# Optimization experiments

Measured on AMD Instinct MI355X. Metric: run time of the kernel, lower is better.

Reference implementation:

```python
import jax, jax.numpy as jnp
import numpy as np

HIDDEN = 1280
HEADS = 16
HEAD_DIM = HIDDEN // HEADS  # 80
TOTAL = 8192
N_CHUNKS = 8


def rotate_half(x):
    x1, x2 = jnp.split(x, 2, axis=-1)
    return jnp.concatenate([-x2, x1], axis=-1)


def setup_inputs() -> dict:
    key = jax.random.key(0)
    ks = jax.random.split(key, 7)
    hidden_states = jax.random.normal(ks[0], (TOTAL, HIDDEN), dtype=jnp.float32)
    cos = jax.random.uniform(ks[1], (TOTAL, HEAD_DIM), dtype=jnp.float32)
    sin = jax.random.uniform(ks[2], (TOTAL, HEAD_DIM), dtype=jnp.float32)
    s = 1.0 / np.sqrt(HIDDEN)
    w_qkv = jax.random.normal(ks[3], (HIDDEN, 3 * HIDDEN), dtype=jnp.float32) * s
    b_qkv = jax.random.normal(ks[4], (3 * HIDDEN,), dtype=jnp.float32) * 0.01
    w_proj = jax.random.normal(ks[5], (HIDDEN, HIDDEN), dtype=jnp.float32) * s
    b_proj = jax.random.normal(ks[6], (HIDDEN,), dtype=jnp.float32) * 0.01
    return {"hidden_states": hidden_states, "cos": cos, "sin": sin,
            "w_qkv": w_qkv, "b_qkv": b_qkv, "w_proj": w_proj,
            "b_proj": b_proj, "n_chunks": N_CHUNKS}


def reference(hidden_states, cos, sin, w_qkv, b_qkv, w_proj, b_proj, n_chunks):
    T, D = hidden_states.shape
    C = int(n_chunks)
    L = T // C  # equal-length chunks (block-diagonal varlen attention)
    H, hd = HEADS, HEAD_DIM
    scale = hd ** -0.5

    qkv = hidden_states @ w_qkv + b_qkv                    # [T, 3D]
    q, k, v = jnp.split(qkv, 3, axis=-1)
    # [C, L, H, hd]
    q = q.reshape(C, L, H, hd)
    k = k.reshape(C, L, H, hd)
    v = v.reshape(C, L, H, hd)
    cos_c = cos.reshape(C, L, 1, hd)
    sin_c = sin.reshape(C, L, 1, hd)
    q = q * cos_c + rotate_half(q) * sin_c
    k = k * cos_c + rotate_half(k) * sin_c

    # block-diagonal attention: each chunk attends only within itself
    scores = jnp.einsum('clhd,cmhd->chlm', q, k) * scale   # [C, H, L, L]
    weights = jax.nn.softmax(scores.astype(jnp.float32), axis=-1).astype(v.dtype)
    attn = jnp.einsum('chlm,cmhd->clhd', weights, v)       # [C, L, H, hd]
    attn = attn.reshape(T, D)
    return attn @ w_proj + b_proj
```

## Files before the change

### kernel.cpp

```cpp
#include <hip/hip_runtime.h>

#define T_TOK 8192
#define D_HID 1280
#define H_    16
#define HD_   80
#define C_    8
#define L_    1024
#define N3_   3840
#define QPAD  96

typedef _Float16 f16;
typedef __attribute__((ext_vector_type(8))) _Float16 h8;
typedef __attribute__((ext_vector_type(4))) float f32x4;

__global__ __launch_bounds__(256) void convert_x(const float* __restrict__ x,
                                                 f16* __restrict__ y) {
  const int g = blockIdx.x * 256 + threadIdx.x;
  const float4 v = ((const float4*)x)[g];
  f16 o[4] = {(f16)v.x, (f16)v.y, (f16)v.z, (f16)v.w};
  ((uint2*)y)[g] = *(const uint2*)o;
}

__global__ __launch_bounds__(256) void convert_w_t(const float* __restrict__ W,
                                                   f16* __restrict__ Wt,
                                                   int K, int N) {
  __shared__ float tile[32][33];
  const int n0 = blockIdx.x * 32, k0 = blockIdx.y * 32;
  const int c = threadIdx.x & 31, r0 = threadIdx.x >> 5;
#pragma unroll
  for (int it = 0; it < 4; ++it) {
    const int r = r0 + it * 8;
    tile[r][c] = W[(size_t)(k0 + r) * N + n0 + c];
  }
  __syncthreads();
#pragma unroll
  for (int it = 0; it < 4; ++it) {
    const int r = r0 + it * 8;
    Wt[(size_t)(n0 + r) * K + k0 + c] = (f16)tile[c][r];
  }
}

__device__ __forceinline__ void stage_rows(const f16* __restrict__ gbase, int K,
                                           f16* sdst, int nchunks, int tid) {
  for (int s0 = 0; s0 < nchunks; s0 += 256) {
    const int s = s0 + tid;
    const int row = s >> 3;
    const int part = (s & 7) ^ (row & 7);
    const f16* gp = gbase + (size_t)row * K + part * 8;
    __builtin_amdgcn_global_load_lds(
        (const __attribute__((address_space(1))) void*)gp,
        (__attribute__((address_space(3))) void*)(sdst + s * 8),
        16, 0, 0);
  }
}

__device__ __forceinline__ h8 fragld64(const f16* s, int row, int c) {
  const int slot = c ^ (row & 7);
  return *(const h8*)&s[row * 64 + slot * 8];
}

__global__ __launch_bounds__(256, 2) void gemm_f16(
    const f16* __restrict__ A, const f16* __restrict__ B,
    const float* __restrict__ bias,
    float* __restrict__ Cf, f16* __restrict__ Ch,
    int M, int N, int K) {
  __shared__ f16 sA[128 * 64], sB[256 * 64];
  const int tid = threadIdx.x;
  const int wave = tid >> 6, lane = tid & 63;
  const int quad = lane >> 4, ln = lane & 15;
  const int bm = blockIdx.y * 128, bn = blockIdx.x * 256;
  const int wm = (wave >> 1) * 64, wn = (wave & 1) * 128;

  f32x4 acc[4][8];
#pragma unroll
  for (int i = 0; i < 4; ++i)
#pragma unroll
    for (int j = 0; j < 8; ++j) acc[i][j] = (f32x4){0.f, 0.f, 0.f, 0.f};

  for (int k0 = 0; k0 < K; k0 += 64) {
    __syncthreads();
    stage_rows(A + (size_t)bm * K + k0, K, sA, 128 * 8, tid);
    stage_rows(B + (size_t)bn * K + k0, K, sB, 256 * 8, tid);
    __syncthreads();

#pragma unroll
    for (int ks = 0; ks < 2; ++ks) {
      h8 af[4], bf[8];
#pragma unroll
      for (int i = 0; i < 4; ++i) af[i] = fragld64(sA, wm + i * 16 + ln, ks * 4 + quad);
#pragma unroll
      for (int j = 0; j < 8; ++j) bf[j] = fragld64(sB, wn + j * 16 + ln, ks * 4 + quad);
#pragma unroll
      for (int i = 0; i < 4; ++i)
#pragma unroll
        for (int j = 0; j < 8; ++j)
          acc[i][j] = __builtin_amdgcn_mfma_f32_16x16x32_f16(af[i], bf[j], acc[i][j], 0, 0, 0);
    }
  }

  float bv[8];
#pragma unroll
  for (int j = 0; j < 8; ++j) bv[j] = bias[bn + wn + j * 16 + ln];
#pragma unroll
  for (int i = 0; i < 4; ++i)
#pragma unroll
    for (int j = 0; j < 8; ++j)
#pragma unroll
      for (int r = 0; r < 4; ++r) {
        const int row = bm + wm + i * 16 + quad * 4 + r;
        const int col = bn + wn + j * 16 + ln;
        const float val = acc[i][j][r] + bv[j];
        if (Ch) Ch[(size_t)row * N + col] = (f16)val;
        else    Cf[(size_t)row * N + col] = val;
      }
}

__global__ __launch_bounds__(256) void rope_convert(
    const f16* __restrict__ qkv, const float* __restrict__ cosb,
    const float* __restrict__ sinb, f16* __restrict__ Qb, f16* __restrict__ Kb) {
  const int tid = threadIdx.x;
  const int wave = tid >> 6, lane = tid & 63;
  const int t = blockIdx.x * 4 + wave;
  const size_t rowb = (size_t)t * N3_;
  const float qscale = 0.11180339887498949f;
#pragma unroll
  for (int u = 0; u < 5; ++u) {
    const int g = u * 64 + lane;
    const int e = g * 8;
    const int d = e % HD_;
    const int h = (e % D_HID) / HD_;
    const bool isK = e >= D_HID;
    const bool lo = d < 40;
    const int pe = lo ? e + 40 : e - 40;
    f16 v[8], p[8];
    *(int4*)v = *(const int4*)(qkv + rowb + e);
    *(int4*)p = *(const int4*)(qkv + rowb + pe);
    const float4 cs0 = *(const float4*)(cosb + (size_t)t * HD_ + d);
    const float4 cs1 = *(const float4*)(cosb + (size_t)t * HD_ + d + 4);
    const float4 sn0 = *(const float4*)(sinb + (size_t)t * HD_ + d);
    const float4 sn1 = *(const float4*)(sinb + (size_t)t * HD_ + d + 4);
    const float cs[8] = {cs0.x, cs0.y, cs0.z, cs0.w, cs1.x, cs1.y, cs1.z, cs1.w};
    const float sn[8] = {sn0.x, sn0.y, sn0.z, sn0.w, sn1.x, sn1.y, sn1.z, sn1.w};
    f16 o[8];
#pragma unroll
    for (int j = 0; j < 8; ++j) {
      const float pv = lo ? -(float)p[j] : (float)p[j];
      const float ov = (float)v[j] * cs[j] + pv * sn[j];
      o[j] = (f16)(isK ? ov : ov * qscale);
    }
    *(int4*)((isK ? Kb : Qb) + ((size_t)h * T_TOK + t) * QPAD + d) = *(const int4*)o;
  }
  {
    const int qk = lane >> 5, h = (lane >> 1) & 15, half = lane & 1;
    f16* dst = (qk ? Kb : Qb) + ((size_t)h * T_TOK + t) * QPAD + 80 + half * 8;
    *(int4*)dst = make_int4(0, 0, 0, 0);
  }
}

__global__ __launch_bounds__(256) void vt_convert(const f16* __restrict__ qkv,
                                                  f16* __restrict__ Vt) {
  __shared__ f16 tl[HD_][136];
  const int h = blockIdx.x & 15;
  const int t0 = (blockIdx.x >> 4) * 128;
  const int tid = threadIdx.x;
#pragma unroll
  for (int it = 0; it < 5; ++it) {
    const int e = tid + it * 256;
    const int t = e / 10, pc = e % 10;
    int4 v = *(const int4*)(qkv + (size_t)(t0 + t) * N3_ + 2 * D_HID + h * HD_ + pc * 8);
    f16 tmp[8];
    *(int4*)tmp = v;
#pragma unroll
    for (int u = 0; u < 8; ++u) tl[pc * 8 + u][t] = tmp[u];
  }
  __syncthreads();
#pragma unroll
  for (int it = 0; it < 5; ++it) {
    const int e = tid + it * 256;
    const int d = e >> 4, pt = e & 15;
    *(int4*)(Vt + ((size_t)h * HD_ + d) * T_TOK + t0 + pt * 8) = *(const int4*)&tl[d][pt * 8];
  }
}

__global__ __launch_bounds__(256, 2) void attn_flash(
    const f16* __restrict__ Qb, const f16* __restrict__ Kb,
    const f16* __restrict__ Vt, f16* __restrict__ Oa) {
  __shared__ f16 Ps[4][64][72];
  const int tid = threadIdx.x;
  const int wave = tid >> 6, lane = tid & 63;
  const int quad = lane >> 4, ln = lane & 15;
  const int h = blockIdx.x & 15;
  const int qb = (blockIdx.x >> 4) & 3;
  const int c = blockIdx.x >> 6;
  const int t0 = c * L_ + qb * 256 + wave * 64;
  const size_t hb = (size_t)h * T_TOK;

  h8 aq[4][3];
#pragma unroll
  for (int i = 0; i < 4; ++i)
#pragma unroll
    for (int ks = 0; ks < 3; ++ks)
      aq[i][ks] = *(const h8*)(Qb + (hb + t0 + i * 16 + ln) * QPAD + ks * 32 + quad * 8);

  f32x4 o[4][5];
  float lsum[4][4];
#pragma unroll
  for (int i = 0; i < 4; ++i) {
#pragma unroll
    for (int jn = 0; jn < 5; ++jn) o[i][jn] = (f32x4){0.f, 0.f, 0.f, 0.f};
#pragma unroll
    for (int r = 0; r < 4; ++r) lsum[i][r] = 0.f;
  }

  for (int kb = 0; kb < 16; ++kb) {
    const int kt0 = c * L_ + kb * 64;
#pragma unroll
    for (int j = 0; j < 4; ++j) {
      h8 bk[3];
#pragma unroll
      for (int ks = 0; ks < 3; ++ks)
        bk[ks] = *(const h8*)(Kb + (hb + kt0 + j * 16 + ln) * QPAD + ks * 32 + quad * 8);
      f32x4 s[4];
#pragma unroll
      for (int i = 0; i < 4; ++i) s[i] = (f32x4){0.f, 0.f, 0.f, 0.f};
      __builtin_amdgcn_s_setprio(1);
#pragma unroll
      for (int ks = 0; ks < 3; ++ks)
#pragma unroll
        for (int i = 0; i < 4; ++i)
          s[i] = __builtin_amdgcn_mfma_f32_16x16x32_f16(aq[i][ks], bk[ks], s[i], 0, 0, 0);
      __builtin_amdgcn_s_setprio(0);
#pragma unroll
      for (int i = 0; i < 4; ++i)
#pragma unroll
        for (int r = 0; r < 4; ++r) {
          const float p = __expf(s[i][r]);
          lsum[i][r] += p;
          Ps[wave][i * 16 + quad * 4 + r][j * 16 + ln] = (f16)p;
        }
    }
#pragma unroll
    for (int ks = 0; ks < 2; ++ks) {
      h8 ap[4];
#pragma unroll
      for (int i = 0; i < 4; ++i)
        ap[i] = *(const h8*)&Ps[wave][i * 16 + ln][ks * 32 + quad * 8];
#pragma unroll
      for (int jn = 0; jn < 5; ++jn) {
        const h8 bv = *(const h8*)(Vt + ((size_t)h * HD_ + jn * 16 + ln) * T_TOK
                                   + kt0 + ks * 32 + quad * 8);
        __builtin_amdgcn_s_setprio(1);
#pragma unroll
        for (int i = 0; i < 4; ++i)
          o[i][jn] = __builtin_amdgcn_mfma_f32_16x16x32_f16(ap[i], bv, o[i][jn], 0, 0, 0);
        __builtin_amdgcn_s_setprio(0);
      }
    }
  }

#pragma unroll
  for (int i = 0; i < 4; ++i)
#pragma unroll
    for (int r = 0; r < 4; ++r) {
      float s = lsum[i][r];
#pragma unroll
      for (int off = 1; off < 16; off <<= 1) s += __shfl_xor(s, off);
      lsum[i][r] = 1.f / s;
    }

#pragma unroll
  for (int i = 0; i < 4; ++i)
#pragma unroll
    for (int r = 0; r < 4; ++r) {
      const int t = t0 + i * 16 + quad * 4 + r;
      const float inv = lsum[i][r];
#pragma unroll
      for (int jn = 0; jn < 5; ++jn)
        Oa[(size_t)t * D_HID + h * HD_ + jn * 16 + ln] = (f16)(o[i][jn][r] * inv);
    }
}

extern "C" void kernel_launch(void* const* d_in, const int* in_sizes, int n_in,
                              void* d_out, int out_size, void* d_ws, size_t ws_size,
                              hipStream_t stream) {
  (void)in_sizes; (void)n_in; (void)out_size; (void)ws_size;
  const float* x      = (const float*)d_in[0];
  const float* cosb   = (const float*)d_in[1];
  const float* sinb   = (const float*)d_in[2];
  const float* w_qkv  = (const float*)d_in[3];
  const float* b_qkv  = (const float*)d_in[4];
  const float* w_proj = (const float*)d_in[5];
  const float* b_proj = (const float*)d_in[6];
  float* out = (float*)d_out;

  char* ws = (char*)d_ws;
  f16* qkv_h  = (f16*)(ws);
  f16* attn_h = (f16*)(ws);
  f16* x_h    = (f16*)(ws + 62914560);
  f16* Qb     = (f16*)(ws + 62914560);
  f16* Kb     = (f16*)(ws + 88080384);
  f16* Vt     = (f16*)(ws + 113246208);
  f16* wq_t   = (f16*)(ws + 134217728);
  f16* wp_t   = (f16*)(ws + 144048128);

  convert_x<<<(T_TOK * D_HID / 4) / 256, 256, 0, stream>>>(x, x_h);
  convert_w_t<<<dim3(N3_ / 32, D_HID / 32), 256, 0, stream>>>(w_qkv, wq_t, D_HID, N3_);
  convert_w_t<<<dim3(D_HID / 32, D_HID / 32), 256, 0, stream>>>(w_proj, wp_t, D_HID, D_HID);
  gemm_f16<<<dim3(N3_ / 256, T_TOK / 128), 256, 0, stream>>>(
      x_h, wq_t, b_qkv, nullptr, qkv_h, T_TOK, N3_, D_HID);
  rope_convert<<<T_TOK / 4, 256, 0, stream>>>(qkv_h, cosb, sinb, Qb, Kb);
  vt_convert<<<H_ * (T_TOK / 128), 256, 0, stream>>>(qkv_h, Vt);
  attn_flash<<<C_ * 4 * H_, 256, 0, stream>>>(Qb, Kb, Vt, attn_h);
  gemm_f16<<<dim3(D_HID / 256, T_TOK / 128), 256, 0, stream>>>(
      attn_h, wp_t, b_proj, out, nullptr, T_TOK, D_HID, D_HID);
}
```

Baseline: 376.2 us.

## Double-buffer GEMM LDS with 256x256 tiles, 512 threads and XCD-aware block remap

Restructures the f16 GEMM to use 256x256 output tiles with 8 waves, double-buffered LDS staging via global_load_lds, and partial vmcnt waits. The next K-tile now loads while the current one runs through MFMA, so the kernel no longer stalls on every barrier. Blocks are remapped across the 8 XCDs to improve L2 locality, and s_setprio is raised around the MFMA bursts. The cost is 128KB of LDS per block, which limits occupancy. The hand-written waitcnt counts depend on the exact number of staging loads, so they are fragile if that count changes.

```diff
diff --git a/kernel.cpp b/kernel.cpp
--- a/kernel.cpp
+++ b/kernel.cpp
@@ -40,9 +40,10 @@
   }
 }
 
-__device__ __forceinline__ void stage_rows(const f16* __restrict__ gbase, int K,
-                                           f16* sdst, int nchunks, int tid) {
-  for (int s0 = 0; s0 < nchunks; s0 += 256) {
+__device__ __forceinline__ void stage_rows512(const f16* __restrict__ gbase, int K,
+                                              f16* sdst, int tid) {
+#pragma unroll
+  for (int s0 = 0; s0 < 2048; s0 += 512) {
     const int s = s0 + tid;
     const int row = s >> 3;
     const int part = (s & 7) ^ (row & 7);
@@ -59,52 +60,74 @@
   return *(const h8*)&s[row * 64 + slot * 8];
 }
 
-__global__ __launch_bounds__(256, 2) void gemm_f16(
+__global__ __launch_bounds__(512, 2) void gemm_f16(
     const f16* __restrict__ A, const f16* __restrict__ B,
     const float* __restrict__ bias,
     float* __restrict__ Cf, f16* __restrict__ Ch,
     int M, int N, int K) {
-  __shared__ f16 sA[128 * 64], sB[256 * 64];
+  __shared__ f16 sAB[2][2][256 * 64];
   const int tid = threadIdx.x;
   const int wave = tid >> 6, lane = tid & 63;
   const int quad = lane >> 4, ln = lane & 15;
-  const int bm = blockIdx.y * 128, bn = blockIdx.x * 256;
-  const int wm = (wave >> 1) * 64, wn = (wave & 1) * 128;
-
-  f32x4 acc[4][8];
-#pragma unroll
-  for (int i = 0; i < 4; ++i)
-#pragma unroll
-    for (int j = 0; j < 8; ++j) acc[i][j] = (f32x4){0.f, 0.f, 0.f, 0.f};
-
-  for (int k0 = 0; k0 < K; k0 += 64) {
-    __syncthreads();
-    stage_rows(A + (size_t)bm * K + k0, K, sA, 128 * 8, tid);
-    stage_rows(B + (size_t)bn * K + k0, K, sB, 256 * 8, tid);
-    __syncthreads();
-
+
+  const int nwg = gridDim.x;
+  int wg = blockIdx.x;
+  wg = (wg & 7) * (nwg >> 3) + (wg >> 3);
+  const int nbx = N >> 8;
+  const int bm = (wg / nbx) * 256, bn = (wg % nbx) * 256;
+  const int wm = (wave >> 2) * 128, wn = (wave & 3) * 64;
+
+  f32x4 acc[8][4];
+#pragma unroll
+  for (int i = 0; i < 8; ++i)
+#pragma unroll
+    for (int j = 0; j < 4; ++j) acc[i][j] = (f32x4){0.f, 0.f, 0.f, 0.f};
+
+  const f16* Abase = A + (size_t)bm * K;
+  const f16* Bbase = B + (size_t)bn * K;
+
+  stage_rows512(Abase, K, sAB[0][0], tid);
+  stage_rows512(Bbase, K, sAB[0][1], tid);
+
+  const int nt = K >> 6;
+  for (int t = 0; t < nt; ++t) {
+    if (t + 1 < nt) {
+      stage_rows512(Abase + (t + 1) * 64, K, sAB[(t + 1) & 1][0], tid);
+      stage_rows512(Bbase + (t + 1) * 64, K, sAB[(t + 1) & 1][1], tid);
+      asm volatile("s_waitcnt vmcnt(8)" ::: "memory");
+    } else {
+      asm volatile("s_waitcnt vmcnt(0)" ::: "memory");
+    }
+    __builtin_amdgcn_sched_barrier(0);
+    __builtin_amdgcn_s_barrier();
+
+    const f16* sA = sAB[t & 1][0];
+    const f16* sB = sAB[t & 1][1];
 #pragma unroll
     for (int ks = 0; ks < 2; ++ks) {
-      h8 af[4], bf[8];
-#pragma unroll
-      for (int i = 0; i < 4; ++i) af[i] = fragld64(sA, wm + i * 16 + ln, ks * 4 + quad);
-#pragma unroll
-      for (int j = 0; j < 8; ++j) bf[j] = fragld64(sB, wn + j * 16 + ln, ks * 4 + quad);
-#pragma unroll
-      for (int i = 0; i < 4; ++i)
-#pragma unroll
-        for (int j = 0; j < 8; ++j)
+      h8 af[8], bf[4];
+#pragma unroll
+      for (int i = 0; i < 8; ++i) af[i] = fragld64(sA, wm + i * 16 + ln, ks * 4 + quad);
+#pragma unroll
+      for (int j = 0; j < 4; ++j) bf[j] = fragld64(sB, wn + j * 16 + ln, ks * 4 + quad);
+      __builtin_amdgcn_s_setprio(1);
+#pragma unroll
+      for (int i = 0; i < 8; ++i)
+#pragma unroll
+        for (int j = 0; j < 4; ++j)
           acc[i][j] = __builtin_amdgcn_mfma_f32_16x16x32_f16(af[i], bf[j], acc[i][j], 0, 0, 0);
-    }
-  }
-
-  float bv[8];
-#pragma unroll
-  for (int j = 0; j < 8; ++j) bv[j] = bias[bn + wn + j * 16 + ln];
-#pragma unroll
-  for (int i = 0; i < 4; ++i)
-#pragma unroll
-    for (int j = 0; j < 8; ++j)
+      __builtin_amdgcn_s_setprio(0);
+    }
+    __builtin_amdgcn_s_barrier();
+  }
+
+  float bv[4];
+#pragma unroll
+  for (int j = 0; j < 4; ++j) bv[j] = bias[bn + wn + j * 16 + ln];
+#pragma unroll
+  for (int i = 0; i < 8; ++i)
+#pragma unroll
+    for (int j = 0; j < 4; ++j)
 #pragma unroll
       for (int r = 0; r < 4; ++r) {
         const int row = bm + wm + i * 16 + quad * 4 + r;
@@ -306,11 +329,11 @@
   convert_x<<<(T_TOK * D_HID / 4) / 256, 256, 0, stream>>>(x, x_h);
   convert_w_t<<<dim3(N3_ / 32, D_HID / 32), 256, 0, stream>>>(w_qkv, wq_t, D_HID, N3_);
   convert_w_t<<<dim3(D_HID / 32, D_HID / 32), 256, 0, stream>>>(w_proj, wp_t, D_HID, D_HID);
-  gemm_f16<<<dim3(N3_ / 256, T_TOK / 128), 256, 0, stream>>>(
+  gemm_f16<<<(N3_ / 256) * (T_TOK / 256), 512, 0, stream>>>(
       x_h, wq_t, b_qkv, nullptr, qkv_h, T_TOK, N3_, D_HID);
   rope_convert<<<T_TOK / 4, 256, 0, stream>>>(qkv_h, cosb, sinb, Qb, Kb);
   vt_convert<<<H_ * (T_TOK / 128), 256, 0, stream>>>(qkv_h, Vt);
   attn_flash<<<C_ * 4 * H_, 256, 0, stream>>>(Qb, Kb, Vt, attn_h);
-  gemm_f16<<<dim3(D_HID / 256, T_TOK / 128), 256, 0, stream>>>(
+  gemm_f16<<<(D_HID / 256) * (T_TOK / 256), 512, 0, stream>>>(
       attn_h, wp_t, b_proj, out, nullptr, T_TOK, D_HID, D_HID);
 }
```

Result: no change. 375.8 us (-0.1%).
